# Kernel optimization log

Measured on AMD Instinct MI355X. Metric: run time of the kernel, lower is better.

## Reference

```python
import jax, jax.numpy as jnp
import numpy as np
import math

D_MODEL = 512
N_HEADS = 8
HEAD_DIM = D_MODEL // N_HEADS


def setup_inputs() -> dict:
    key = jax.random.key(0)
    k1, k2, k3 = jax.random.split(key, 3)
    B, T = 2, 4096
    x = jax.random.normal(k1, (B, T, D_MODEL), dtype=jnp.float32)
    # nn.Linear weights: stored as [out, in], applied as x @ W.T
    W_QKV = jax.random.normal(k2, (3 * D_MODEL, D_MODEL), dtype=jnp.float32) * (1.0 / math.sqrt(D_MODEL))
    W_O = jax.random.normal(k3, (D_MODEL, D_MODEL), dtype=jnp.float32) * (1.0 / math.sqrt(D_MODEL))
    return {"x": x, "W_QKV": W_QKV, "W_O": W_O}


def reference(x, W_QKV, W_O):
    B, T, C = x.shape
    qkv = (x @ W_QKV.T).reshape(B, T, 3, N_HEADS, HEAD_DIM)
    q, k, v = qkv[:, :, 0], qkv[:, :, 1], qkv[:, :, 2]  # [B,T,H,D]
    # scores: [B,H,T,T]
    scale = math.sqrt(HEAD_DIM)
    attn = jnp.einsum('bqhd,bkhd->bhqk', q, k) / scale
    causal_mask = jnp.triu(jnp.ones((T, T), dtype=bool), k=1)
    attn = jnp.where(causal_mask, -jnp.inf, attn)
    attn = jax.nn.softmax(attn, axis=-1)
    out = jnp.einsum('bhqk,bkhd->bqhd', attn, v).reshape(B, T, C)
    return out @ W_O.T
```

## Files before the change

kernel.cpp:

```cpp
#include <hip/hip_runtime.h>
#include <hip/hip_bf16.h>

typedef __bf16 bf16_t;
typedef __bf16 bf16x8 __attribute__((ext_vector_type(8)));
typedef __bf16 bf16x4 __attribute__((ext_vector_type(4)));
typedef float  floatx4 __attribute__((ext_vector_type(4)));

static __device__ __forceinline__ floatx4 mfma16(bf16x8 a, bf16x8 b, floatx4 c) {
  return __builtin_amdgcn_mfma_f32_16x16x32_bf16(a, b, c, 0, 0, 0);
}

typedef __attribute__((address_space(3))) void lds_vp;
typedef __attribute__((address_space(1))) void glb_vp;
#define GLDS16(g, l) \
  __builtin_amdgcn_global_load_lds((glb_vp*)(g), (lds_vp*)(l), 16, 0, 0)

__global__ void cvt_all_kernel(const float* __restrict__ x,
                               const float* __restrict__ wqkv,
                               const float* __restrict__ wo,
                               bf16_t* __restrict__ xb,
                               bf16_t* __restrict__ wqkvb,
                               bf16_t* __restrict__ wob) {
  int i = blockIdx.x * blockDim.x + threadIdx.x;
  const float4* src; bf16x4* dst; int off;
  if (i < 1048576)      { src = (const float4*)x;    dst = (bf16x4*)xb;    off = i; }
  else if (i < 1245184) { src = (const float4*)wqkv; dst = (bf16x4*)wqkvb; off = i - 1048576; }
  else                  { src = (const float4*)wo;   dst = (bf16x4*)wob;   off = i - 1245184; }
  float4 v = src[off];
  bf16x4 o;
  o[0] = (bf16_t)v.x; o[1] = (bf16_t)v.y; o[2] = (bf16_t)v.z; o[3] = (bf16_t)v.w;
  dst[off] = o;
}

__global__ __launch_bounds__(256) void gemm_qkv(
    const bf16_t* __restrict__ A, const bf16_t* __restrict__ B,
    bf16_t* __restrict__ Qo, bf16_t* __restrict__ Ko, bf16_t* __restrict__ Vto)
{
  __shared__ __align__(16) bf16_t As[2][128 * 64];
  __shared__ __align__(16) bf16_t Bs[2][128 * 64];
  const int tid  = threadIdx.x;
  const int lane = tid & 63;
  const int w    = tid >> 6;
  const int quad = lane >> 4;
  const int l15  = lane & 15;
  const int l7   = lane & 7;
  const int wm   = w & 1;
  const int wn   = w >> 1;
  const int K    = 512;

  floatx4 acc[4][4];
  #pragma unroll
  for (int i = 0; i < 4; ++i)
    #pragma unroll
    for (int j = 0; j < 4; ++j)
      acc[i][j] = (floatx4){0.f, 0.f, 0.f, 0.f};

  const bf16_t* Ab = A + (size_t)blockIdx.x * 128 * K;
  const bf16_t* Bb = B + (size_t)blockIdx.y * 128 * K;

  auto stage = [&](int buf, int k0) {
    #pragma unroll
    for (int i = 0; i < 4; ++i) {
      int c = tid + 256 * i;
      int row = c >> 3, colc = c & 7;
      int gofs = ((colc ^ (row & 7)) << 3);
      GLDS16(&Ab[(size_t)row * K + k0 + gofs], &As[buf][c * 8]);
      GLDS16(&Bb[(size_t)row * K + k0 + gofs], &Bs[buf][c * 8]);
    }
  };

  stage(0, 0);
  for (int it = 0; it < 8; ++it) {
    const int cur = it & 1;
    __syncthreads();
    if (it + 1 < 8) stage(cur ^ 1, (it + 1) << 6);
    #pragma unroll
    for (int ks = 0; ks < 2; ++ks) {
      bf16x8 af[4], bfr[4];
      #pragma unroll
      for (int t = 0; t < 4; ++t) {
        af[t]  = *(const bf16x8*)&As[cur][(wm * 64 + t * 16 + l15) * 64 +
                                         (((ks * 4 + quad) ^ l7) << 3)];
        bfr[t] = *(const bf16x8*)&Bs[cur][(wn * 64 + t * 16 + l15) * 64 +
                                         (((ks * 4 + quad) ^ l7) << 3)];
      }
      #pragma unroll
      for (int mt = 0; mt < 4; ++mt)
        #pragma unroll
        for (int nt = 0; nt < 4; ++nt)
          acc[mt][nt] = mfma16(af[mt], bfr[nt], acc[mt][nt]);
    }
  }

  if (blockIdx.y < 8) {
    #pragma unroll
    for (int mt = 0; mt < 4; ++mt) {
      #pragma unroll
      for (int nt = 0; nt < 4; ++nt) {
        #pragma unroll
        for (int r = 0; r < 4; ++r) {
          int m = blockIdx.x * 128 + wm * 64 + mt * 16 + quad * 4 + r;
          int n = blockIdx.y * 128 + wn * 64 + nt * 16 + l15;
          float v = acc[mt][nt][r];
          int b = m >> 12, t = m & 4095;
          int h = (n >> 6) & 7, d = n & 63;
          size_t bh = (size_t)(b * 8 + h);
          if (n < 512)
            Qo[bh * 262144 + (size_t)t * 64 + d] = (bf16_t)(v * 0.18033688f);
          else
            Ko[bh * 262144 +
               (size_t)((((t >> 4) * 2 + (d >> 5)) * 512) +
                        ((((d & 31) >> 3) * 16 + (t & 15)) * 8) + (d & 7))] =
                (bf16_t)v;
        }
      }
    }
  } else {
    __syncthreads();
    bf16_t* L = &As[0][0];
    #pragma unroll
    for (int mt = 0; mt < 4; ++mt)
      #pragma unroll
      for (int nt = 0; nt < 4; ++nt) {
        int n_l = wn * 64 + nt * 16 + l15;
        int mc  = wm * 8 + mt * 2 + (quad >> 1);
        bf16x4 v4;
        #pragma unroll
        for (int r = 0; r < 4; ++r) v4[r] = (bf16_t)acc[mt][nt][r];
        *(bf16x4*)&L[n_l * 128 + ((mc ^ (n_l & 15)) << 3) + (quad & 1) * 4] = v4;
      }
    __syncthreads();
    const int t0 = (blockIdx.x & 31) * 128;
    const int b  = blockIdx.x >> 5;
    #pragma unroll
    for (int i = 0; i < 8; ++i) {
      int c = tid + 256 * i;
      int n_l = c >> 4, tc = c & 15;
      int h = ((blockIdx.y - 8) << 1) | (n_l >> 6);
      int d = n_l & 63;
      size_t bh = (size_t)(b * 8 + h);
      int base0 = (tc >> 2) * 32 + (tc & 3) * 4;
      bf16x4 lo = *(const bf16x4*)&L[n_l * 128 +
                     (((base0 >> 3) ^ (n_l & 15)) << 3) + (base0 & 7)];
      bf16x4 hi = *(const bf16x4*)&L[n_l * 128 +
                     ((((base0 + 16) >> 3) ^ (n_l & 15)) << 3) + (base0 & 7)];
      bf16x8 o;
      #pragma unroll
      for (int e = 0; e < 4; ++e) { o[e] = lo[e]; o[e + 4] = hi[e]; }
      int T = t0 + tc * 8;
      *(bf16x8*)&Vto[bh * 262144 +
                     (size_t)((((T >> 5) * 4 + (d >> 4)) * 512) +
                              ((((T >> 3) & 3) * 16 + (d & 15)) * 8))] = o;
    }
  }
}

__global__ __launch_bounds__(256) void gemm_out(
    const bf16_t* __restrict__ A, const bf16_t* __restrict__ B,
    float* __restrict__ Cf)
{
  __shared__ __align__(16) bf16_t As[2][64 * 64];
  __shared__ __align__(16) bf16_t Bs[2][128 * 64];
  const int tid  = threadIdx.x;
  const int lane = tid & 63;
  const int w    = tid >> 6;
  const int quad = lane >> 4;
  const int l15  = lane & 15;
  const int l7   = lane & 7;

  floatx4 acc[4][2];
  #pragma unroll
  for (int i = 0; i < 4; ++i)
    #pragma unroll
    for (int j = 0; j < 2; ++j)
      acc[i][j] = (floatx4){0.f, 0.f, 0.f, 0.f};

  const bf16_t* Ab = A + (size_t)blockIdx.x * 64 * 512;
  const bf16_t* Bb = B + (size_t)blockIdx.y * 128 * 512;

  auto stage = [&](int buf, int k0) {
    #pragma unroll
    for (int i = 0; i < 2; ++i) {
      int c = tid + 256 * i;
      int row = c >> 3, colc = c & 7;
      GLDS16(&Ab[(size_t)row * 512 + k0 + ((colc ^ (row & 7)) << 3)],
             &As[buf][c * 8]);
    }
    #pragma unroll
    for (int i = 0; i < 4; ++i) {
      int c = tid + 256 * i;
      int row = c >> 3, colc = c & 7;
      GLDS16(&Bb[(size_t)row * 512 + k0 + ((colc ^ (row & 7)) << 3)],
             &Bs[buf][c * 8]);
    }
  };

  stage(0, 0);
  for (int it = 0; it < 8; ++it) {
    const int cur = it & 1;
    __syncthreads();
    if (it + 1 < 8) stage(cur ^ 1, (it + 1) << 6);
    #pragma unroll
    for (int ks = 0; ks < 2; ++ks) {
      bf16x8 af[4], bfr[2];
      #pragma unroll
      for (int t = 0; t < 4; ++t)
        af[t]  = *(const bf16x8*)&As[cur][(t * 16 + l15) * 64 +
                                         (((ks * 4 + quad) ^ l7) << 3)];
      #pragma unroll
      for (int t = 0; t < 2; ++t)
        bfr[t] = *(const bf16x8*)&Bs[cur][(w * 32 + t * 16 + l15) * 64 +
                                         (((ks * 4 + quad) ^ l7) << 3)];
      #pragma unroll
      for (int mt = 0; mt < 4; ++mt)
        #pragma unroll
        for (int nt = 0; nt < 2; ++nt)
          acc[mt][nt] = mfma16(af[mt], bfr[nt], acc[mt][nt]);
    }
  }

  #pragma unroll
  for (int mt = 0; mt < 4; ++mt)
    #pragma unroll
    for (int nt = 0; nt < 2; ++nt)
      #pragma unroll
      for (int r = 0; r < 4; ++r) {
        int m = blockIdx.x * 64 + mt * 16 + quad * 4 + r;
        int n = blockIdx.y * 128 + w * 32 + nt * 16 + l15;
        Cf[(size_t)m * 512 + n] = acc[mt][nt][r];
      }
}

__global__ __launch_bounds__(512, 1) void attn_kernel(
    const bf16_t* __restrict__ Qg, const bf16_t* __restrict__ Kf,
    const bf16_t* __restrict__ Vf, bf16_t* __restrict__ Og)
{
  __shared__ __align__(16) bf16_t smem[49664];

  const int tid  = threadIdx.x;
  const int lane = tid & 63;
  const int w    = tid >> 6;
  const int tile = w >> 2;
  const int qh   = (w >> 1) & 1;
  const int kh   = w & 1;
  const int quad = lane >> 4;
  const int l15  = lane & 15;

  const int id = blockIdx.x;
  const int bh = 2 * (id & 7) + ((id >> 3) & 1);
  const int x  = id >> 4;
  const int qtA = 31 - x, qtB = x;
  const int qt  = tile ? qtB : qtA;
  const int q64 = 2 * qt + qh;
  const size_t bh_off = (size_t)bh * 262144;
  const int b = bh >> 3, h = bh & 7;

  const int qbase = qt * 128 + qh * 64;
  bf16x8 aq0[4], aq1[4];
  #pragma unroll
  for (int qb = 0; qb < 4; ++qb) {
    const bf16_t* Qp = Qg + bh_off + (size_t)(qbase + qb * 16 + l15) * 64;
    aq0[qb] = *(const bf16x8*)&Qp[quad * 8];
    aq1[qb] = *(const bf16x8*)&Qp[32 + quad * 8];
  }
  bf16x8 ones;
  #pragma unroll
  for (int i = 0; i < 8; ++i) ones[i] = (bf16_t)1.0f;

  floatx4 acc_o[4][4], acc_l[4];
  #pragma unroll
  for (int qb = 0; qb < 4; ++qb) {
    #pragma unroll
    for (int dt = 0; dt < 4; ++dt) acc_o[qb][dt] = (floatx4){0.f, 0.f, 0.f, 0.f};
    acc_l[qb] = (floatx4){0.f, 0.f, 0.f, 0.f};
  }

  const bf16_t* Kb_ = Kf + bh_off;
  const bf16_t* Vb_ = Vf + bh_off;
  const floatx4 z4 = (floatx4){0.f, 0.f, 0.f, 0.f};

  for (int k64 = kh; k64 <= q64; k64 += 2) {
    const bf16_t* Kp = Kb_ + (size_t)k64 * 4096;
    const bf16_t* Vp = Vb_ + (size_t)k64 * 4096;
    bf16x8 bk0[4], bk1[4];
    #pragma unroll
    for (int nt = 0; nt < 4; ++nt) {
      bk0[nt] = *(const bf16x8*)&Kp[(nt * 2 + 0) * 512 + lane * 8];
      bk1[nt] = *(const bf16x8*)&Kp[(nt * 2 + 1) * 512 + lane * 8];
    }
    floatx4 s[4][4];
    #pragma unroll
    for (int nt = 0; nt < 4; ++nt) {
      s[0][nt] = mfma16(bk0[nt], aq0[0], z4);
      s[1][nt] = mfma16(bk0[nt], aq0[1], z4);
      s[2][nt] = mfma16(bk0[nt], aq0[2], z4);
      s[3][nt] = mfma16(bk0[nt], aq0[3], z4);
    }
    #pragma unroll
    for (int nt = 0; nt < 4; ++nt)
      #pragma unroll
      for (int qb = 0; qb < 4; ++qb)
        s[qb][nt] = mfma16(bk1[nt], aq1[qb], s[qb][nt]);
    bf16x8 av[2][4];
    #pragma unroll
    for (int kc = 0; kc < 2; ++kc)
      #pragma unroll
      for (int dt = 0; dt < 4; ++dt)
        av[kc][dt] = *(const bf16x8*)&Vp[(kc * 4 + dt) * 512 + lane * 8];
    if (k64 == q64) {
      #pragma unroll
      for (int qb = 0; qb < 4; ++qb)
        #pragma unroll
        for (int nt = 0; nt < 4; ++nt)
          #pragma unroll
          for (int r = 0; r < 4; ++r)
            if (nt * 16 + quad * 4 + r > qb * 16 + l15)
              s[qb][nt][r] = -3.0e38f;
    }
    #pragma unroll
    for (int qb = 0; qb < 4; ++qb)
      #pragma unroll
      for (int nt = 0; nt < 4; ++nt)
        #pragma unroll
        for (int r = 0; r < 4; ++r)
          s[qb][nt][r] = __builtin_amdgcn_exp2f(s[qb][nt][r]);
    #pragma unroll
    for (int kc = 0; kc < 2; ++kc) {
      bf16x8 pb[4];
      #pragma unroll
      for (int qb = 0; qb < 4; ++qb)
        #pragma unroll
        for (int r = 0; r < 4; ++r) {
          pb[qb][r]     = (bf16_t)s[qb][kc * 2][r];
          pb[qb][r + 4] = (bf16_t)s[qb][kc * 2 + 1][r];
        }
      #pragma unroll
      for (int qb = 0; qb < 4; ++qb)
        acc_l[qb] = mfma16(ones, pb[qb], acc_l[qb]);
      #pragma unroll
      for (int dt = 0; dt < 4; ++dt)
        #pragma unroll
        for (int qb = 0; qb < 4; ++qb)
          acc_o[qb][dt] = mfma16(av[kc][dt], pb[qb], acc_o[qb][dt]);
    }
  }

  __syncthreads();
  float*  PART = (float*)smem;
  bf16_t* OUT  = smem + 33280;
  const int p = w >> 1;
  float* P = PART + p * 4160;

  if (kh == 1) {
    #pragma unroll
    for (int qb = 0; qb < 4; ++qb) {
      #pragma unroll
      for (int dt = 0; dt < 4; ++dt) {
        int chunk = (dt * 4 + quad) ^ l15;
        *(floatx4*)&P[(qb * 16 + l15) * 64 + chunk * 4] = acc_o[qb][dt];
      }
      if (quad == 0) P[4096 + qb * 16 + l15] = acc_l[qb][0];
    }
  }
  __syncthreads();
  if (kh == 0) {
    bf16_t* Ot = OUT + p * 4096;
    #pragma unroll
    for (int qb = 0; qb < 4; ++qb) {
      const int t_own = qb * 16 + l15;
      float rl = 1.0f / (acc_l[qb][0] + P[4096 + t_own]);
      #pragma unroll
      for (int dt = 0; dt < 4; ++dt) {
        int chunk = (dt * 4 + quad) ^ l15;
        floatx4 pp = *(const floatx4*)&P[t_own * 64 + chunk * 4];
        bf16x4 o4;
        #pragma unroll
        for (int r = 0; r < 4; ++r)
          o4[r] = (bf16_t)((acc_o[qb][dt][r] + pp[r]) * rl);
        *(bf16x4*)&Ot[t_own * 64 +
                      (((dt * 2 + (quad >> 1)) ^ (t_own & 7)) << 3) +
                      (quad & 1) * 4] = o4;
      }
    }
  }
  __syncthreads();
  {
    bf16_t* Ot = OUT + p * 4096;
    const int gtid = ((w & 1) << 6) | lane;
    #pragma unroll
    for (int i = 0; i < 4; ++i) {
      int cc = gtid + 128 * i;
      int t = cc >> 3, c = cc & 7;
      bf16x8 o8 = *(const bf16x8*)&Ot[t * 64 + ((c ^ (t & 7)) << 3)];
      int trow = qbase + t;
      *(bf16x8*)&Og[((size_t)b * 4096 + trow) * 512 + h * 64 + c * 8] = o8;
    }
  }
}

extern "C" void kernel_launch(void* const* d_in, const int* in_sizes, int n_in,
                              void* d_out, int out_size, void* d_ws, size_t ws_size,
                              hipStream_t stream) {
  const float* x    = (const float*)d_in[0];
  const float* wqkv = (const float*)d_in[1];
  const float* wo   = (const float*)d_in[2];
  float* out = (float*)d_out;

  char* ws = (char*)d_ws;
  bf16_t* xb    = (bf16_t*)(ws);
  bf16_t* wqkvb = (bf16_t*)(ws + 8388608);
  bf16_t* wob   = (bf16_t*)(ws + 9961472);
  bf16_t* Qb    = (bf16_t*)(ws + 10485760);
  bf16_t* Kfb   = (bf16_t*)(ws + 18874368);
  bf16_t* Vfb   = (bf16_t*)(ws + 27262976);
  bf16_t* Ob    = xb;

  cvt_all_kernel<<<5120, 256, 0, stream>>>(x, wqkv, wo, xb, wqkvb, wob);

  gemm_qkv<<<dim3(64, 12), 256, 0, stream>>>(xb, wqkvb, Qb, Kfb, Vfb);
  attn_kernel<<<dim3(256), 512, 0, stream>>>(Qb, Kfb, Vfb, Ob);
  gemm_out<<<dim3(128, 4), 256, 0, stream>>>(Ob, wob, out);
}
```

Before: 148.1 us.

## Split attention key range across four waves per query block, process tiles sequentially

Each block used to run two query tiles at once on separate warp groups, with a two-way key split. Now all eight waves work on one query tile at a time, two query halves times a four-way key split, and the block handles the long and short tiles in two sequential phases. Partial outputs and row sums go to a larger LDS area and are reduced by all threads before writing bf16 output. The aim is to balance causal work better across waves and shorten the longest wave's key loop, at the cost of more LDS, an extra reduction and barriers per phase.

Result: faster. 144.8 us (-2.2%).

```diff
diff --git a/kernel.cpp b/kernel.cpp
--- a/kernel.cpp
+++ b/kernel.cpp
@@ -235,14 +235,13 @@
     const bf16_t* __restrict__ Qg, const bf16_t* __restrict__ Kf,
     const bf16_t* __restrict__ Vf, bf16_t* __restrict__ Og)
 {
-  __shared__ __align__(16) bf16_t smem[49664];
+  __shared__ __align__(16) bf16_t smem[66560];
 
   const int tid  = threadIdx.x;
   const int lane = tid & 63;
   const int w    = tid >> 6;
-  const int tile = w >> 2;
-  const int qh   = (w >> 1) & 1;
-  const int kh   = w & 1;
+  const int qh   = w >> 2;
+  const int kq   = w & 3;
   const int quad = lane >> 4;
   const int l15  = lane & 15;
 
@@ -250,151 +249,142 @@
   const int bh = 2 * (id & 7) + ((id >> 3) & 1);
   const int x  = id >> 4;
   const int qtA = 31 - x, qtB = x;
-  const int qt  = tile ? qtB : qtA;
-  const int q64 = 2 * qt + qh;
   const size_t bh_off = (size_t)bh * 262144;
   const int b = bh >> 3, h = bh & 7;
 
-  const int qbase = qt * 128 + qh * 64;
-  bf16x8 aq0[4], aq1[4];
-  #pragma unroll
-  for (int qb = 0; qb < 4; ++qb) {
-    const bf16_t* Qp = Qg + bh_off + (size_t)(qbase + qb * 16 + l15) * 64;
-    aq0[qb] = *(const bf16x8*)&Qp[quad * 8];
-    aq1[qb] = *(const bf16x8*)&Qp[32 + quad * 8];
-  }
+  const bf16_t* Kb_ = Kf + bh_off;
+  const bf16_t* Vb_ = Vf + bh_off;
+  const floatx4 z4 = (floatx4){0.f, 0.f, 0.f, 0.f};
   bf16x8 ones;
   #pragma unroll
   for (int i = 0; i < 8; ++i) ones[i] = (bf16_t)1.0f;
 
-  floatx4 acc_o[4][4], acc_l[4];
-  #pragma unroll
-  for (int qb = 0; qb < 4; ++qb) {
-    #pragma unroll
-    for (int dt = 0; dt < 4; ++dt) acc_o[qb][dt] = (floatx4){0.f, 0.f, 0.f, 0.f};
-    acc_l[qb] = (floatx4){0.f, 0.f, 0.f, 0.f};
-  }
-
-  const bf16_t* Kb_ = Kf + bh_off;
-  const bf16_t* Vb_ = Vf + bh_off;
-  const floatx4 z4 = (floatx4){0.f, 0.f, 0.f, 0.f};
-
-  for (int k64 = kh; k64 <= q64; k64 += 2) {
-    const bf16_t* Kp = Kb_ + (size_t)k64 * 4096;
-    const bf16_t* Vp = Vb_ + (size_t)k64 * 4096;
-    bf16x8 bk0[4], bk1[4];
-    #pragma unroll
-    for (int nt = 0; nt < 4; ++nt) {
-      bk0[nt] = *(const bf16x8*)&Kp[(nt * 2 + 0) * 512 + lane * 8];
-      bk1[nt] = *(const bf16x8*)&Kp[(nt * 2 + 1) * 512 + lane * 8];
-    }
-    floatx4 s[4][4];
-    #pragma unroll
-    for (int nt = 0; nt < 4; ++nt) {
-      s[0][nt] = mfma16(bk0[nt], aq0[0], z4);
-      s[1][nt] = mfma16(bk0[nt], aq0[1], z4);
-      s[2][nt] = mfma16(bk0[nt], aq0[2], z4);
-      s[3][nt] = mfma16(bk0[nt], aq0[3], z4);
-    }
-    #pragma unroll
-    for (int nt = 0; nt < 4; ++nt)
-      #pragma unroll
-      for (int qb = 0; qb < 4; ++qb)
-        s[qb][nt] = mfma16(bk1[nt], aq1[qb], s[qb][nt]);
-    bf16x8 av[2][4];
-    #pragma unroll
-    for (int kc = 0; kc < 2; ++kc)
-      #pragma unroll
-      for (int dt = 0; dt < 4; ++dt)
-        av[kc][dt] = *(const bf16x8*)&Vp[(kc * 4 + dt) * 512 + lane * 8];
-    if (k64 == q64) {
+  for (int ph = 0; ph < 2; ++ph) {
+    const int qt   = ph ? qtB : qtA;
+    const int q64  = 2 * qt + qh;
+    const int qbase = qt * 128 + qh * 64;
+
+    bf16x8 aq0[4], aq1[4];
+    #pragma unroll
+    for (int qb = 0; qb < 4; ++qb) {
+      const bf16_t* Qp = Qg + bh_off + (size_t)(qbase + qb * 16 + l15) * 64;
+      aq0[qb] = *(const bf16x8*)&Qp[quad * 8];
+      aq1[qb] = *(const bf16x8*)&Qp[32 + quad * 8];
+    }
+
+    floatx4 acc_o[4][4], acc_l[4];
+    #pragma unroll
+    for (int qb = 0; qb < 4; ++qb) {
+      #pragma unroll
+      for (int dt = 0; dt < 4; ++dt) acc_o[qb][dt] = (floatx4){0.f, 0.f, 0.f, 0.f};
+      acc_l[qb] = (floatx4){0.f, 0.f, 0.f, 0.f};
+    }
+
+    for (int k64 = kq; k64 <= q64; k64 += 4) {
+      const bf16_t* Kp = Kb_ + (size_t)k64 * 4096;
+      const bf16_t* Vp = Vb_ + (size_t)k64 * 4096;
+      bf16x8 bk0[4], bk1[4];
+      #pragma unroll
+      for (int nt = 0; nt < 4; ++nt) {
+        bk0[nt] = *(const bf16x8*)&Kp[(nt * 2 + 0) * 512 + lane * 8];
+        bk1[nt] = *(const bf16x8*)&Kp[(nt * 2 + 1) * 512 + lane * 8];
+      }
+      floatx4 s[4][4];
+      #pragma unroll
+      for (int nt = 0; nt < 4; ++nt) {
+        s[0][nt] = mfma16(bk0[nt], aq0[0], z4);
+        s[1][nt] = mfma16(bk0[nt], aq0[1], z4);
+        s[2][nt] = mfma16(bk0[nt], aq0[2], z4);
+        s[3][nt] = mfma16(bk0[nt], aq0[3], z4);
+      }
+      #pragma unroll
+      for (int nt = 0; nt < 4; ++nt)
+        #pragma unroll
+        for (int qb = 0; qb < 4; ++qb)
+          s[qb][nt] = mfma16(bk1[nt], aq1[qb], s[qb][nt]);
+      bf16x8 av[2][4];
+      #pragma unroll
+      for (int kc = 0; kc < 2; ++kc)
+        #pragma unroll
+        for (int dt = 0; dt < 4; ++dt)
+          av[kc][dt] = *(const bf16x8*)&Vp[(kc * 4 + dt) * 512 + lane * 8];
+      if (k64 == q64) {
+        #pragma unroll
+        for (int qb = 0; qb < 4; ++qb)
+          #pragma unroll
+          for (int nt = 0; nt < 4; ++nt)
+            #pragma unroll
+            for (int r = 0; r < 4; ++r)
+              if (nt * 16 + quad * 4 + r > qb * 16 + l15)
+                s[qb][nt][r] = -3.0e38f;
+      }
       #pragma unroll
       for (int qb = 0; qb < 4; ++qb)
         #pragma unroll
         for (int nt = 0; nt < 4; ++nt)
           #pragma unroll
           for (int r = 0; r < 4; ++r)
-            if (nt * 16 + quad * 4 + r > qb * 16 + l15)
-              s[qb][nt][r] = -3.0e38f;
-    }
-    #pragma unroll
-    for (int qb = 0; qb < 4; ++qb)
-      #pragma unroll
-      for (int nt = 0; nt < 4; ++nt)
-        #pragma unroll
-        for (int r = 0; r < 4; ++r)
-          s[qb][nt][r] = __builtin_amdgcn_exp2f(s[qb][nt][r]);
-    #pragma unroll
-    for (int kc = 0; kc < 2; ++kc) {
-      bf16x8 pb[4];
-      #pragma unroll
-      for (int qb = 0; qb < 4; ++qb)
-        #pragma unroll
-        for (int r = 0; r < 4; ++r) {
-          pb[qb][r]     = (bf16_t)s[qb][kc * 2][r];
-          pb[qb][r + 4] = (bf16_t)s[qb][kc * 2 + 1][r];
-        }
-      #pragma unroll
-      for (int qb = 0; qb < 4; ++qb)
-        acc_l[qb] = mfma16(ones, pb[qb], acc_l[qb]);
-      #pragma unroll
-      for (int dt = 0; dt < 4; ++dt)
+            s[qb][nt][r] = __builtin_amdgcn_exp2f(s[qb][nt][r]);
+      #pragma unroll
+      for (int kc = 0; kc < 2; ++kc) {
+        bf16x8 pb[4];
         #pragma unroll
         for (int qb = 0; qb < 4; ++qb)
-          acc_o[qb][dt] = mfma16(av[kc][dt], pb[qb], acc_o[qb][dt]);
-    }
-  }
-
-  __syncthreads();
-  float*  PART = (float*)smem;
-  bf16_t* OUT  = smem + 33280;
-  const int p = w >> 1;
-  float* P = PART + p * 4160;
-
-  if (kh == 1) {
-    #pragma unroll
-    for (int qb = 0; qb < 4; ++qb) {
-      #pragma unroll
-      for (int dt = 0; dt < 4; ++dt) {
-        int chunk = (dt * 4 + quad) ^ l15;
-        *(floatx4*)&P[(qb * 16 + l15) * 64 + chunk * 4] = acc_o[qb][dt];
-      }
-      if (quad == 0) P[4096 + qb * 16 + l15] = acc_l[qb][0];
-    }
-  }
-  __syncthreads();
-  if (kh == 0) {
-    bf16_t* Ot = OUT + p * 4096;
-    #pragma unroll
-    for (int qb = 0; qb < 4; ++qb) {
-      const int t_own = qb * 16 + l15;
-      float rl = 1.0f / (acc_l[qb][0] + P[4096 + t_own]);
-      #pragma unroll
-      for (int dt = 0; dt < 4; ++dt) {
-        int chunk = (dt * 4 + quad) ^ l15;
-        floatx4 pp = *(const floatx4*)&P[t_own * 64 + chunk * 4];
-        bf16x4 o4;
-        #pragma unroll
-        for (int r = 0; r < 4; ++r)
-          o4[r] = (bf16_t)((acc_o[qb][dt][r] + pp[r]) * rl);
-        *(bf16x4*)&Ot[t_own * 64 +
-                      (((dt * 2 + (quad >> 1)) ^ (t_own & 7)) << 3) +
-                      (quad & 1) * 4] = o4;
-      }
-    }
-  }
-  __syncthreads();
-  {
-    bf16_t* Ot = OUT + p * 4096;
-    const int gtid = ((w & 1) << 6) | lane;
-    #pragma unroll
-    for (int i = 0; i < 4; ++i) {
-      int cc = gtid + 128 * i;
-      int t = cc >> 3, c = cc & 7;
-      bf16x8 o8 = *(const bf16x8*)&Ot[t * 64 + ((c ^ (t & 7)) << 3)];
-      int trow = qbase + t;
-      *(bf16x8*)&Og[((size_t)b * 4096 + trow) * 512 + h * 64 + c * 8] = o8;
-    }
+          #pragma unroll
+          for (int r = 0; r < 4; ++r) {
+            pb[qb][r]     = (bf16_t)s[qb][kc * 2][r];
+            pb[qb][r + 4] = (bf16_t)s[qb][kc * 2 + 1][r];
+          }
+        #pragma unroll
+        for (int qb = 0; qb < 4; ++qb)
+          acc_l[qb] = mfma16(ones, pb[qb], acc_l[qb]);
+        #pragma unroll
+        for (int dt = 0; dt < 4; ++dt)
+          #pragma unroll
+          for (int qb = 0; qb < 4; ++qb)
+            acc_o[qb][dt] = mfma16(av[kc][dt], pb[qb], acc_o[qb][dt]);
+      }
+    }
+
+    {
+      float* Pq = (float*)&smem[0] + (qh * 4 + kq) * 4096;
+      float* PL = (float*)&smem[65536];
+      #pragma unroll
+      for (int qb = 0; qb < 4; ++qb) {
+        int q = qb * 16 + l15;
+        #pragma unroll
+        for (int dt = 0; dt < 4; ++dt)
+          *(floatx4*)&Pq[q * 64 + (((dt * 4 + quad) ^ l15) << 2)] = acc_o[qb][dt];
+        if (quad == 0) PL[(qh * 4 + kq) * 64 + q] = acc_l[qb][0];
+      }
+    }
+    __syncthreads();
+    #pragma unroll
+    for (int i = 0; i < 2; ++i) {
+      int a = tid + 512 * i;
+      int qh_e = a >> 9, rem = a & 511;
+      int q = rem >> 3, c8 = rem & 7;
+      const float* Pq = (const float*)&smem[0] + qh_e * 16384;
+      const float* PL = (const float*)&smem[65536] + qh_e * 256;
+      float s0[8] = {0.f, 0.f, 0.f, 0.f, 0.f, 0.f, 0.f, 0.f};
+      float suml = 0.f;
+      #pragma unroll
+      for (int k2 = 0; k2 < 4; ++k2) {
+        const float* Pk = Pq + k2 * 4096 + q * 64;
+        floatx4 u0 = *(const floatx4*)&Pk[((c8 * 2)     ^ (q & 15)) << 2];
+        floatx4 u1 = *(const floatx4*)&Pk[((c8 * 2 + 1) ^ (q & 15)) << 2];
+        #pragma unroll
+        for (int r = 0; r < 4; ++r) { s0[r] += u0[r]; s0[4 + r] += u1[r]; }
+        suml += PL[k2 * 64 + q];
+      }
+      float rl = 1.0f / suml;
+      bf16x8 o;
+      #pragma unroll
+      for (int e = 0; e < 8; ++e) o[e] = (bf16_t)(s0[e] * rl);
+      int row = qt * 128 + qh_e * 64 + q;
+      *(bf16x8*)&Og[((size_t)b * 4096 + row) * 512 + h * 64 + c8 * 8] = o;
+    }
+    if (ph == 0) __syncthreads();
   }
 }
 
```
